# Kernel tuning notes

Measured on AMD Instinct MI355X. Metric: run time of the kernel, lower is better.

The kernel has to match this reference:

```python
import jax, jax.numpy as jnp
import numpy as np

N = 50000
E = 800000
D = 128
L = 3
EPS = 1e-5


def setup_inputs() -> dict:
    key = jax.random.key(0)
    ks = jax.random.split(key, 8)
    x = jax.random.normal(ks[0], (N, D), dtype=jnp.float32)
    edge_index = jax.random.randint(ks[1], (2, E), 0, N, dtype=jnp.int64)
    s = 1.0 / np.sqrt(D)
    # stacked per-layer params (all layers are 128->128)
    Wl = jax.random.uniform(ks[2], (L, D, D), jnp.float32, -s, s)  # lin_l weight
    bl = jax.random.uniform(ks[3], (L, D), jnp.float32, -s, s)     # lin_l bias
    Wr = jax.random.uniform(ks[4], (L, D, D), jnp.float32, -s, s)  # lin_r weight (no bias)
    gamma = jnp.ones((L, D), jnp.float32)
    beta = jnp.zeros((L, D), jnp.float32)
    return {"x": x, "edge_index": edge_index, "Wl": Wl, "bl": bl,
            "Wr": Wr, "gamma": gamma, "beta": beta}


def layer_norm(h, g, b):
    mu = jnp.mean(h, axis=-1, keepdims=True)
    var = jnp.mean(jnp.square(h - mu), axis=-1, keepdims=True)
    return (h - mu) * jax.lax.rsqrt(var + EPS) * g + b


def reference(x, edge_index, Wl, bl, Wr, gamma, beta):
    src = edge_index[0]
    dst = edge_index[1]
    # in-degree counts (constant wrt features)
    cnt = jax.ops.segment_sum(jnp.ones((E,), jnp.float32), dst, num_segments=N)
    inv_cnt = (1.0 / jnp.maximum(cnt, 1.0))[:, None]  # [N,1]
    h = x
    for l in range(L):
        # mean neighbor aggregation: gather source feats, scatter-add to dst
        agg = jax.ops.segment_sum(h[src], dst, num_segments=N) * inv_cnt
        # SAGEConv: lin_l(agg) + lin_r(h)
        h2 = agg @ Wl[l].T + bl[l] + h @ Wr[l].T
        h2 = layer_norm(h2, gamma[l], beta[l])
        h = jax.nn.relu(h2)  # dropout is identity at inference
    return h
```

## Files before the change

### kernel.cpp

```cpp
#include <hip/hip_runtime.h>
#include <hip/hip_bf16.h>
#include <stdint.h>

#define NN 50000
#define EE 800000
#define DD 128
#define LL 3

typedef __attribute__((ext_vector_type(8))) short short8;
typedef __attribute__((ext_vector_type(4))) float float4v;

__device__ __forceinline__ float bf2f(unsigned int u) {
  union { unsigned int i; float f; } x; x.i = u << 16; return x.f;
}
__device__ __forceinline__ unsigned short f2bf(float f) {
  union { float f; unsigned int i; } x; x.f = f;
  unsigned int r = x.i + 0x7FFFu + ((x.i >> 16) & 1u);
  return (unsigned short)(r >> 16);
}

__global__ void deg_kernel(const int* __restrict__ dst, int* __restrict__ deg, int E) {
  int e = blockIdx.x * blockDim.x + threadIdx.x;
  if (e < E) atomicAdd(&deg[dst[e]], 1);
}

__global__ __launch_bounds__(256) void scan1_kernel(
    const int* __restrict__ deg, int* __restrict__ incl, int* __restrict__ partial, int N) {
  __shared__ int wsums[4];
  const int tid = threadIdx.x, lane = tid & 63, wid = tid >> 6;
  int i = blockIdx.x * 256 + tid;
  int v = (i < N) ? deg[i] : 0;
  int x = v;
#pragma unroll
  for (int off = 1; off < 64; off <<= 1) {
    int y = __shfl_up(x, off, 64);
    if (lane >= off) x += y;
  }
  if (lane == 63) wsums[wid] = x;
  __syncthreads();
  if (tid == 0) {
    int a0 = wsums[0], a1 = wsums[1], a2 = wsums[2];
    wsums[0] = 0; wsums[1] = a0; wsums[2] = a0 + a1; wsums[3] = a0 + a1 + a2;
  }
  __syncthreads();
  int inc = wsums[wid] + x;
  if (i < N) incl[i] = inc;
  if (tid == 255) partial[blockIdx.x] = inc;
}

__global__ __launch_bounds__(256) void scan2_kernel(int* __restrict__ partial, int P) {
  __shared__ int wsums[4];
  const int tid = threadIdx.x, lane = tid & 63, wid = tid >> 6;
  int v = (tid < P) ? partial[tid] : 0;
  int x = v;
#pragma unroll
  for (int off = 1; off < 64; off <<= 1) {
    int y = __shfl_up(x, off, 64);
    if (lane >= off) x += y;
  }
  if (lane == 63) wsums[wid] = x;
  __syncthreads();
  if (tid == 0) {
    int a0 = wsums[0], a1 = wsums[1], a2 = wsums[2];
    wsums[0] = 0; wsums[1] = a0; wsums[2] = a0 + a1; wsums[3] = a0 + a1 + a2;
  }
  __syncthreads();
  int excl = wsums[wid] + x - v;
  if (tid < P) partial[tid] = excl;
}

__global__ __launch_bounds__(256) void scan3_kernel(
    const int* __restrict__ incl, const int* __restrict__ deg, const int* __restrict__ partial,
    int* __restrict__ rowptr, int* __restrict__ cursor, int N) {
  int i = blockIdx.x * 256 + threadIdx.x;
  if (i < N) {
    int rp = incl[i] - deg[i] + partial[blockIdx.x];
    rowptr[i] = rp;
    cursor[i] = rp;
  }
  if (i == 0) rowptr[N] = EE;
}

__global__ void fill_kernel(const int* __restrict__ src, const int* __restrict__ dst,
                            int* __restrict__ cursor, int* __restrict__ col, int E) {
  int e = blockIdx.x * blockDim.x + threadIdx.x;
  if (e < E) {
    int d = dst[e];
    int pos = atomicAdd(&cursor[d], 1);
    col[pos] = src[e];
  }
}

__global__ void convert_kernel(const float* __restrict__ x, unsigned short* __restrict__ hbf, int n4) {
  int i = blockIdx.x * blockDim.x + threadIdx.x;
  if (i < n4) {
    float4 v = ((const float4*)x)[i];
    ushort4 o;
    o.x = f2bf(v.x); o.y = f2bf(v.y); o.z = f2bf(v.z); o.w = f2bf(v.w);
    ((ushort4*)hbf)[i] = o;
  }
}

__global__ void repack_kernel(const float* __restrict__ Wl, const float* __restrict__ Wr,
                              unsigned short* __restrict__ out) {
  int tid = blockIdx.x * blockDim.x + threadIdx.x;
  if (tid >= LL * 8 * 8 * 64) return;
  int lane = tid & 63;
  int t = (tid >> 6) & 7;
  int ks = (tid >> 9) & 7;
  int l = tid >> 12;
  int n = t * 16 + (lane & 15);
  int kbase = ks * 32 + (lane >> 4) * 8;
  const float* Wsrc = (ks < 4) ? (Wl + ((size_t)(l * 128 + n) * 128 + kbase))
                               : (Wr + ((size_t)(l * 128 + n) * 128 + (kbase - 128)));
#pragma unroll
  for (int j = 0; j < 8; j++) out[(size_t)tid * 8 + j] = f2bf(Wsrc[j]);
}

__global__ __launch_bounds__(256) void agg_kernel(
    const unsigned short* __restrict__ hbf, const int* __restrict__ rowptr,
    const int* __restrict__ col, unsigned short* __restrict__ agg, int N) {
  int node = blockIdx.x * 4 + (threadIdx.x >> 6);
  if (node >= N) return;
  int lane = threadIdx.x & 63;
  int s = rowptr[node], e = rowptr[node + 1];
  float ax = 0.f, ay = 0.f;
  int i = s;
  for (; i + 7 < e; i += 8) {
    int idx[8];
#pragma unroll
    for (int j = 0; j < 8; j++) idx[j] = col[i + j];
    unsigned int r[8];
#pragma unroll
    for (int j = 0; j < 8; j++) r[j] = ((const unsigned int*)(hbf + (size_t)idx[j] * 128))[lane];
#pragma unroll
    for (int j = 0; j < 8; j++) {
      ax += bf2f(r[j] & 0xffffu);
      ay += bf2f(r[j] >> 16);
    }
  }
  if (i + 3 < e) {
    int idx[4];
#pragma unroll
    for (int j = 0; j < 4; j++) idx[j] = col[i + j];
    unsigned int r[4];
#pragma unroll
    for (int j = 0; j < 4; j++) r[j] = ((const unsigned int*)(hbf + (size_t)idx[j] * 128))[lane];
#pragma unroll
    for (int j = 0; j < 4; j++) {
      ax += bf2f(r[j] & 0xffffu);
      ay += bf2f(r[j] >> 16);
    }
    i += 4;
  }
  for (; i < e; i++) {
    unsigned int r0 = ((const unsigned int*)(hbf + (size_t)col[i] * 128))[lane];
    ax += bf2f(r0 & 0xffffu);
    ay += bf2f(r0 >> 16);
  }
  int dg = e - s;
  float inv = 1.0f / (float)(dg > 1 ? dg : 1);
  ax *= inv; ay *= inv;
  ((unsigned int*)(agg + (size_t)node * 128))[lane] =
      ((unsigned int)f2bf(ay) << 16) | (unsigned int)f2bf(ax);
}

template <bool LAST>
__global__ __launch_bounds__(256) void gemm_ln_mfma_kernel(
    const unsigned short* __restrict__ agg, const unsigned short* __restrict__ h,
    const unsigned short* __restrict__ Bf, const float* __restrict__ bias,
    const float* __restrict__ gamma, const float* __restrict__ beta,
    unsigned short* __restrict__ out_bf, float* __restrict__ f_out, int N) {
  __shared__ unsigned short Bl[8 * 8 * 512];
  __shared__ float reds[64][16];
  __shared__ float redss[64][16];
  __shared__ float mu_s[64], rs_s[64];
  const int tid = threadIdx.x;
  {
    const uint4* srcB = (const uint4*)Bf;
    uint4* dstB = (uint4*)Bl;
#pragma unroll
    for (int i = 0; i < 16; i++) dstB[tid + i * 256] = srcB[tid + i * 256];
  }
  __syncthreads();
  const int wave = tid >> 6, lane = tid & 63;
  const int ln16 = lane & 15, quad = lane >> 4;
  const int m0 = blockIdx.x * 64 + wave * 16;
  int row_a = m0 + ln16;
  if (row_a > N - 1) row_a = N - 1;
  const size_t aoff = (size_t)row_a * 128 + quad * 8;

  float4v acc[8];
#pragma unroll
  for (int t = 0; t < 8; t++) acc[t] = (float4v)0.f;

#pragma unroll
  for (int ks = 0; ks < 8; ks++) {
    const unsigned short* ap = (ks < 4) ? (agg + aoff + ks * 32) : (h + aoff + (ks - 4) * 32);
    short8 a = *(const short8*)ap;
#pragma unroll
    for (int t = 0; t < 8; t++) {
      short8 b = *(const short8*)&Bl[(ks * 8 + t) * 512 + lane * 8];
      acc[t] = __builtin_amdgcn_mfma_f32_16x16x32_bf16(a, b, acc[t], 0, 0, 0);
    }
  }

  float bias_v[8], g_v[8], b_v[8];
#pragma unroll
  for (int t = 0; t < 8; t++) {
    int c = t * 16 + ln16;
    bias_v[t] = bias[c]; g_v[t] = gamma[c]; b_v[t] = beta[c];
  }
#pragma unroll
  for (int r = 0; r < 4; r++) {
    float s = 0.f, ss = 0.f;
#pragma unroll
    for (int t = 0; t < 8; t++) {
      float val = acc[t][r] + bias_v[t];
      s += val; ss += val * val;
    }
    int rowblk = wave * 16 + quad * 4 + r;
    reds[rowblk][ln16] = s;
    redss[rowblk][ln16] = ss;
  }
  __syncthreads();
  if (tid < 64) {
    float s = 0.f, ss = 0.f;
#pragma unroll
    for (int g = 0; g < 16; g++) { s += reds[tid][g]; ss += redss[tid][g]; }
    float mu = s * (1.0f / 128.0f);
    float var = ss * (1.0f / 128.0f) - mu * mu;
    if (var < 0.f) var = 0.f;
    mu_s[tid] = mu;
    rs_s[tid] = rsqrtf(var + 1e-5f);
  }
  __syncthreads();
#pragma unroll
  for (int r = 0; r < 4; r++) {
    int row = m0 + quad * 4 + r;
    int rowblk = wave * 16 + quad * 4 + r;
    if (row < N) {
      float mu = mu_s[rowblk], rs = rs_s[rowblk];
#pragma unroll
      for (int t = 0; t < 8; t++) {
        float val = acc[t][r] + bias_v[t];
        float y = (val - mu) * rs * g_v[t] + b_v[t];
        y = y > 0.f ? y : 0.f;
        int cidx = t * 16 + ln16;
        if (LAST) {
          f_out[(size_t)row * 128 + cidx] = y;
        } else {
          out_bf[(size_t)row * 128 + cidx] = f2bf(y);
        }
      }
    }
  }
}

extern "C" void kernel_launch(void* const* d_in, const int* in_sizes, int n_in,
                              void* d_out, int out_size, void* d_ws, size_t ws_size,
                              hipStream_t stream) {
  const float* x = (const float*)d_in[0];
  const int* edge = (const int*)d_in[1];
  const float* Wl = (const float*)d_in[2];
  const float* bl = (const float*)d_in[3];
  const float* Wr = (const float*)d_in[4];
  const float* gamma = (const float*)d_in[5];
  const float* beta = (const float*)d_in[6];
  float* out = (float*)d_out;

  const int* srcv = edge;
  const int* dstv = edge + EE;

  char* p = (char*)d_ws;
  auto alloc = [&](size_t bytes) {
    char* r = p;
    p += (bytes + 255) & ~(size_t)255;
    return r;
  };
  const size_t bplane = (size_t)NN * 128 * 2;
  unsigned short* xB = (unsigned short*)alloc(bplane);
  unsigned short* h1B = (unsigned short*)alloc(bplane);
  unsigned short* h2B = (unsigned short*)alloc(bplane);
  unsigned short* agB = (unsigned short*)alloc(bplane);
  unsigned short* BfB = (unsigned short*)alloc((size_t)LL * 32768 * 2);
  int* deg = (int*)alloc((size_t)NN * 4);
  int* incl = (int*)alloc((size_t)NN * 4);
  int* cursor = (int*)alloc((size_t)NN * 4);
  int* rowptr = (int*)alloc((size_t)(NN + 1) * 4);
  int* colarr = (int*)alloc((size_t)EE * 4);
  int* partial = (int*)alloc((size_t)256 * 4);
  if ((size_t)(p - (char*)d_ws) > ws_size) return;

  const int SCAN_BLOCKS = (NN + 255) / 256;

  hipMemsetAsync(deg, 0, (size_t)NN * 4, stream);
  deg_kernel<<<(EE + 255) / 256, 256, 0, stream>>>(dstv, deg, EE);
  scan1_kernel<<<SCAN_BLOCKS, 256, 0, stream>>>(deg, incl, partial, NN);
  scan2_kernel<<<1, 256, 0, stream>>>(partial, SCAN_BLOCKS);
  scan3_kernel<<<SCAN_BLOCKS, 256, 0, stream>>>(incl, deg, partial, rowptr, cursor, NN);
  fill_kernel<<<(EE + 255) / 256, 256, 0, stream>>>(srcv, dstv, cursor, colarr, EE);
  convert_kernel<<<(NN * 128 / 4 + 255) / 256, 256, 0, stream>>>(x, xB, NN * 128 / 4);
  repack_kernel<<<(LL * 4096 + 255) / 256, 256, 0, stream>>>(Wl, Wr, BfB);

  const int gemm_grid = (NN + 63) / 64;
  const int agg_grid = (NN + 3) / 4;

  agg_kernel<<<agg_grid, 256, 0, stream>>>(xB, rowptr, colarr, agB, NN);
  gemm_ln_mfma_kernel<false><<<gemm_grid, 256, 0, stream>>>(
      agB, xB, BfB, bl, gamma, beta, h1B, nullptr, NN);

  agg_kernel<<<agg_grid, 256, 0, stream>>>(h1B, rowptr, colarr, agB, NN);
  gemm_ln_mfma_kernel<false><<<gemm_grid, 256, 0, stream>>>(
      agB, h1B, BfB + 32768, bl + 128, gamma + 128, beta + 128, h2B, nullptr, NN);

  agg_kernel<<<agg_grid, 256, 0, stream>>>(h2B, rowptr, colarr, agB, NN);
  gemm_ln_mfma_kernel<true><<<gemm_grid, 256, 0, stream>>>(
      agB, h2B, BfB + 2 * 32768, bl + 256, gamma + 256, beta + 256, nullptr, out, NN);
}
```

Baseline: 314.6 us.

## Partition CSR fill by destination range and deepen aggregation gather unroll

The CSR fill kernel now uses 8 destination-node ranges times 98 edge chunks. Each block scans its whole edge chunk but only inserts edges whose destination falls in its range, so atomics and column writes for a range stay within a narrower part of memory. The aggregation kernel gains a 16-edge unrolled gather stage ahead of the 8-edge stage, putting more loads in flight per wavefront. The costs are that the fill reads dst 8 times over, and the wider unroll raises register pressure.

```diff
diff --git a/kernel.cpp b/kernel.cpp
--- a/kernel.cpp
+++ b/kernel.cpp
@@ -6,6 +6,7 @@
 #define EE 800000
 #define DD 128
 #define LL 3
+#define FILL_CHUNKS 98
 
 typedef __attribute__((ext_vector_type(8))) short short8;
 typedef __attribute__((ext_vector_type(4))) float float4v;
@@ -81,13 +82,22 @@
   if (i == 0) rowptr[N] = EE;
 }
 
-__global__ void fill_kernel(const int* __restrict__ src, const int* __restrict__ dst,
-                            int* __restrict__ cursor, int* __restrict__ col, int E) {
-  int e = blockIdx.x * blockDim.x + threadIdx.x;
-  if (e < E) {
+__global__ __launch_bounds__(256) void fill_kernel(
+    const int* __restrict__ src, const int* __restrict__ dst,
+    int* __restrict__ cursor, int* __restrict__ col, int E) {
+  const int range = blockIdx.x & 7;
+  const int chunk = blockIdx.x >> 3;
+  const int lo = range * (NN / 8);
+  const int hi = lo + (NN / 8);
+  const int per = (E + FILL_CHUNKS - 1) / FILL_CHUNKS;
+  const int e0 = chunk * per;
+  const int e1 = (e0 + per < E) ? (e0 + per) : E;
+  for (int e = e0 + threadIdx.x; e < e1; e += 256) {
     int d = dst[e];
-    int pos = atomicAdd(&cursor[d], 1);
-    col[pos] = src[e];
+    if (d >= lo && d < hi) {
+      int pos = atomicAdd(&cursor[d], 1);
+      col[pos] = src[e];
+    }
   }
 }
 
@@ -126,7 +136,20 @@
   int s = rowptr[node], e = rowptr[node + 1];
   float ax = 0.f, ay = 0.f;
   int i = s;
-  for (; i + 7 < e; i += 8) {
+  for (; i + 15 < e; i += 16) {
+    int idx[16];
+#pragma unroll
+    for (int j = 0; j < 16; j++) idx[j] = col[i + j];
+    unsigned int r[16];
+#pragma unroll
+    for (int j = 0; j < 16; j++) r[j] = ((const unsigned int*)(hbf + (size_t)idx[j] * 128))[lane];
+#pragma unroll
+    for (int j = 0; j < 16; j++) {
+      ax += bf2f(r[j] & 0xffffu);
+      ay += bf2f(r[j] >> 16);
+    }
+  }
+  if (i + 7 < e) {
     int idx[8];
 #pragma unroll
     for (int j = 0; j < 8; j++) idx[j] = col[i + j];
@@ -138,6 +161,7 @@
       ax += bf2f(r[j] & 0xffffu);
       ay += bf2f(r[j] >> 16);
     }
+    i += 8;
   }
   if (i + 3 < e) {
     int idx[4];
@@ -299,7 +323,7 @@
   scan1_kernel<<<SCAN_BLOCKS, 256, 0, stream>>>(deg, incl, partial, NN);
   scan2_kernel<<<1, 256, 0, stream>>>(partial, SCAN_BLOCKS);
   scan3_kernel<<<SCAN_BLOCKS, 256, 0, stream>>>(incl, deg, partial, rowptr, cursor, NN);
-  fill_kernel<<<(EE + 255) / 256, 256, 0, stream>>>(srcv, dstv, cursor, colarr, EE);
+  fill_kernel<<<8 * FILL_CHUNKS, 256, 0, stream>>>(srcv, dstv, cursor, colarr, EE);
   convert_kernel<<<(NN * 128 / 4 + 255) / 256, 256, 0, stream>>>(x, xB, NN * 128 / 4);
   repack_kernel<<<(LL * 4096 + 255) / 256, 256, 0, stream>>>(Wl, Wr, BfB);
 
```

Measured after the change: 305.7 us. 1.03x faster.
